# Kernel optimization log

Hardware: AMD Instinct MI355X
Metric: run time of the kernel (lower is better)

The kernel has to match this reference:

```python
import jax, jax.numpy as jnp
import numpy as np

B, T, F, H = 32, 2048, 768, 12
DH = F // H  # 64


def setup_inputs() -> dict:
    key = jax.random.key(0)
    ks = jax.random.split(key, 4)
    x = jax.random.normal(ks[0], (B, T, F), dtype=jnp.float32)
    mask = jnp.zeros((B, 1, T, 1), dtype=jnp.float32)
    W_attn = jax.random.normal(ks[1], (F, 3 * F), dtype=jnp.float32) * 0.02
    b_attn = jnp.zeros((1, 3 * F), dtype=jnp.float32)
    W_proj = jax.random.normal(ks[2], (F, F), dtype=jnp.float32) * 0.02
    b_proj = jnp.zeros((1, F), dtype=jnp.float32)
    return {"x": x, "mask": mask, "W_attn": W_attn, "b_attn": b_attn,
            "W_proj": W_proj, "b_proj": b_proj}


def _split_heads(t):
    # [B, T, F] -> [B, H, T, dh]
    b, s, f = t.shape
    return t.reshape(b, s, H, f // H).transpose(0, 2, 1, 3)


def _merge_heads(t):
    # [B, H, T, dh] -> [B, T, F]
    b, h, s, d = t.shape
    return t.transpose(0, 2, 1, 3).reshape(b, s, h * d)


def reference(x, mask, W_attn, b_attn, W_proj, b_proj):
    qkv = x @ W_attn + b_attn                      # [B, T, 3F]
    q, k, v = jnp.split(qkv, 3, axis=2)
    q, k, v = _split_heads(q), _split_heads(k), _split_heads(v)  # [B,H,T,dh]

    dk = jnp.asarray(DH, jnp.float32)
    # matmul(q, k, transpose_a=True): contract over T -> [B, H, dh, dh]
    w = jnp.einsum('bhtd,bhte->bhde', q, k) / jnp.sqrt(dk)
    # causal mask over feature axis (nd == ns == dh -> lower triangle)
    i = jnp.arange(DH)[:, None]
    j = jnp.arange(DH)[None, :]
    b = (i >= j).astype(w.dtype)                   # [dh, dh]
    w = w * b - 10000.0 * (1.0 - b)
    # matmul(w, v, transpose_b=True): [B,H,dh,dh] @ [B,H,dh,T] -> [B,H,dh,T]
    w = jnp.einsum('bhde,bhte->bhdt', w, v)
    w = w / (dk ** 4)
    w = w.transpose(0, 1, 3, 2)                    # [B, H, T, dh]
    w = w + mask                                   # mask broadcasts [B,1,T,1]
    w = jax.nn.softmax(w, axis=-2)                 # softmax over time axis
    # dropout is identity at inference (training=False)
    a = v * w                                      # elementwise, not matmul

    a = _merge_heads(a)                            # [B, T, F]
    w = _merge_heads(w)                            # [B, T, F]
    a = a @ W_proj + b_proj
    return (a, w)
```

## Files before the change

### kernel.cpp

```cpp
#include <hip/hip_runtime.h>

#define B_    32
#define T_    2048
#define F_    768
#define H_    12
#define DH_   64
#define MTOK  (B_*T_)
#define NQKV  (3*F_)

typedef __bf16 bf16;
typedef __bf16 bf16x8 __attribute__((ext_vector_type(8)));
typedef float  f32x4  __attribute__((ext_vector_type(4)));

__device__ __forceinline__ void gload_lds16(const bf16* g, bf16* l) {
  __builtin_amdgcn_global_load_lds(
      (const __attribute__((address_space(1))) unsigned*)g,
      (__attribute__((address_space(3))) unsigned*)l, 16, 0, 0);
}

__global__ void k_cast_x(const float* __restrict__ in, bf16* __restrict__ out, int n8) {
  int i = blockIdx.x * 256 + threadIdx.x;
  if (i >= n8) return;
  const float4* p = (const float4*)in + (size_t)i * 2;
  float4 f0 = p[0], f1 = p[1];
  bf16x8 o;
  o[0]=(bf16)f0.x; o[1]=(bf16)f0.y; o[2]=(bf16)f0.z; o[3]=(bf16)f0.w;
  o[4]=(bf16)f1.x; o[5]=(bf16)f1.y; o[6]=(bf16)f1.z; o[7]=(bf16)f1.w;
  *((bf16x8*)out + i) = o;
}

__global__ void k_tcast(const float* __restrict__ in, bf16* __restrict__ out, int K, int N) {
  __shared__ float tile[32][33];
  int n0 = blockIdx.x * 32, k0 = blockIdx.y * 32;
  int tx = threadIdx.x & 31, ty = threadIdx.x >> 5;
#pragma unroll
  for (int r = 0; r < 4; ++r)
    tile[ty + r*8][tx] = in[(size_t)(k0 + ty + r*8) * N + n0 + tx];
  __syncthreads();
#pragma unroll
  for (int r = 0; r < 4; ++r)
    out[(size_t)(n0 + ty + r*8) * K + k0 + tx] = (bf16)tile[tx][ty + r*8];
}

template <typename OutT>
__global__ void k_gemm_bt(const bf16* __restrict__ A, const bf16* __restrict__ Bt,
                          const float* __restrict__ bias, OutT* __restrict__ C,
                          int M, int N, int K, int Nt) {
  __shared__ bf16 As[128 * 32];
  __shared__ bf16 Bs[128 * 32];
  int nwg = gridDim.x;
  int bid = blockIdx.x;
  int swz = (bid & 7) * (nwg >> 3) + (bid >> 3);
  int bn = swz % Nt, bm = swz / Nt;
  int tid = threadIdx.x, wv = tid >> 6, l = tid & 63;
  int wm = (wv >> 1) * 64, wn = (wv & 1) * 64;
  f32x4 acc[4][4] = {};
  const bf16* Ab = A + (size_t)(bm * 128) * K;
  const bf16* Bb = Bt + (size_t)(bn * 128) * K;
  int srow = l >> 2;
  int scol = (l & 3) * 8;
  const int nk = K >> 5;
  for (int kt = 0; kt < nk; ++kt) {
    int k0 = kt * 32;
    __syncthreads();
#pragma unroll
    for (int i = 0; i < 2; ++i) {
      int rr = (i * 4 + wv) * 16 + srow;
      gload_lds16(Ab + (size_t)rr * K + k0 + scol, As + (i * 4 + wv) * 512);
      gload_lds16(Bb + (size_t)rr * K + k0 + scol, Bs + (i * 4 + wv) * 512);
    }
    __syncthreads();
    bf16x8 af[4], bfr[4];
#pragma unroll
    for (int t = 0; t < 4; ++t) {
      af[t]  = *(const bf16x8*)&As[(wm + t * 16 + (l & 15)) * 32 + (l >> 4) * 8];
      bfr[t] = *(const bf16x8*)&Bs[(wn + t * 16 + (l & 15)) * 32 + (l >> 4) * 8];
    }
#pragma unroll
    for (int mi = 0; mi < 4; ++mi)
#pragma unroll
      for (int ni = 0; ni < 4; ++ni)
        acc[mi][ni] = __builtin_amdgcn_mfma_f32_16x16x32_bf16(af[mi], bfr[ni], acc[mi][ni], 0, 0, 0);
  }
#pragma unroll
  for (int ni = 0; ni < 4; ++ni) {
    int col = bn * 128 + wn + ni * 16 + (l & 15);
    float bv = bias[col];
#pragma unroll
    for (int mi = 0; mi < 4; ++mi)
#pragma unroll
      for (int r = 0; r < 4; ++r) {
        int row = bm * 128 + wm + mi * 16 + (l >> 4) * 4 + r;
        C[(size_t)row * N + col] = (OutT)(acc[mi][ni][r] + bv);
      }
  }
}

__global__ __launch_bounds__(256) void k_stage2(const bf16* __restrict__ qkv,
                                                bf16* __restrict__ S2b) {
  int bh = blockIdx.x;
  int b = bh / H_, h = bh % H_;
  int tid = threadIdx.x, wv = tid >> 6, l = tid & 63;
  const bf16* qb = qkv + (size_t)b * T_ * NQKV + h * DH_;
  const bf16* kb = qb + F_;
  f32x4 acc[4][4] = {};
  int tbase = wv * 512 + (l >> 4) * 8;
  int dcol = l & 15;
  for (int kt = 0; kt < 16; ++kt) {
    int t0 = tbase + kt * 32;
    bf16x8 af[4], bfv[4];
#pragma unroll
    for (int j = 0; j < 8; ++j) {
      const bf16* qrow = qb + (size_t)(t0 + j) * NQKV;
      const bf16* krow = kb + (size_t)(t0 + j) * NQKV;
#pragma unroll
      for (int di = 0; di < 4; ++di) {
        af[di][j]  = qrow[di * 16 + dcol];
        bfv[di][j] = krow[di * 16 + dcol];
      }
    }
#pragma unroll
    for (int di = 0; di < 4; ++di)
#pragma unroll
      for (int ej = 0; ej < 4; ++ej)
        acc[di][ej] = __builtin_amdgcn_mfma_f32_16x16x32_bf16(af[di], bfv[ej], acc[di][ej], 0, 0, 0);
  }
  __shared__ float Sred[64][68];
  for (int w = 0; w < 4; ++w) {
    if (wv == w) {
#pragma unroll
      for (int di = 0; di < 4; ++di)
#pragma unroll
        for (int ej = 0; ej < 4; ++ej)
#pragma unroll
          for (int r = 0; r < 4; ++r) {
            int d = di * 16 + (l >> 4) * 4 + r;
            int e = ej * 16 + dcol;
            if (w == 0) Sred[d][e] = acc[di][ej][r];
            else        Sred[d][e] += acc[di][ej][r];
          }
    }
    __syncthreads();
  }
  const float sc_keep = 0.125f / 16777216.0f;
  const float sc_mask = -10000.0f / 16777216.0f;
  bf16* out = S2b + (size_t)bh * 4096;
  for (int i = tid; i < 4096; i += 256) {
    int d = i >> 6, e = i & 63;
    float v = (e <= d) ? Sred[d][e] * sc_keep : sc_mask;
    out[i] = (bf16)v;
  }
}

__global__ __launch_bounds__(256) void k_stage3(const bf16* __restrict__ qkv,
                                                const bf16* __restrict__ S2b,
                                                const float* __restrict__ mask,
                                                float* __restrict__ w_out,
                                                bf16* __restrict__ a_pre) {
  int bh = blockIdx.x;
  int b = bh / H_, h = bh % H_;
  int tid = threadIdx.x, wv = tid >> 6, l = tid & 63;
  const bf16* S2 = S2b + (size_t)bh * 4096;
  bf16x8 sfrag[2][4];
#pragma unroll
  for (int ks = 0; ks < 2; ++ks)
#pragma unroll
    for (int n = 0; n < 4; ++n)
      sfrag[ks][n] = *(const bf16x8*)&S2[(n * 16 + (l & 15)) * 64 + ks * 32 + (l >> 4) * 8];
  const bf16* vb = qkv + (size_t)b * T_ * NQKV + 2 * F_ + h * DH_;
  const float* mb = mask + (size_t)b * T_;
  int t_lo = wv * 512;

  float se[4] = {0.f, 0.f, 0.f, 0.f};
  for (int t0 = t_lo; t0 < t_lo + 512; t0 += 16) {
    f32x4 acc[4] = {};
    bf16x8 a0 = *(const bf16x8*)&vb[(size_t)(t0 + (l & 15)) * NQKV + (l >> 4) * 8];
    bf16x8 a1 = *(const bf16x8*)&vb[(size_t)(t0 + (l & 15)) * NQKV + 32 + (l >> 4) * 8];
#pragma unroll
    for (int n = 0; n < 4; ++n) {
      acc[n] = __builtin_amdgcn_mfma_f32_16x16x32_bf16(a0, sfrag[0][n], acc[n], 0, 0, 0);
      acc[n] = __builtin_amdgcn_mfma_f32_16x16x32_bf16(a1, sfrag[1][n], acc[n], 0, 0, 0);
    }
    float4 mv = *(const float4*)&mb[t0 + (l >> 4) * 4];
    float mr[4] = {mv.x, mv.y, mv.z, mv.w};
#pragma unroll
    for (int n = 0; n < 4; ++n)
#pragma unroll
      for (int r = 0; r < 4; ++r)
        se[n] += __expf(acc[n][r] + mr[r]);
  }
#pragma unroll
  for (int n = 0; n < 4; ++n) {
    se[n] += __shfl_xor(se[n], 16, 64);
    se[n] += __shfl_xor(se[n], 32, 64);
  }
  __shared__ float sred[4][64];
  __shared__ float inv[64];
  if (l < 16) {
#pragma unroll
    for (int n = 0; n < 4; ++n) sred[wv][n * 16 + l] = se[n];
  }
  __syncthreads();
  if (tid < 64) inv[tid] = 1.0f / (sred[0][tid] + sred[1][tid] + sred[2][tid] + sred[3][tid]);
  __syncthreads();
  float iv[4];
#pragma unroll
  for (int n = 0; n < 4; ++n) iv[n] = inv[n * 16 + (l & 15)];

  for (int t0 = t_lo; t0 < t_lo + 512; t0 += 16) {
    f32x4 acc[4] = {};
    bf16x8 a0 = *(const bf16x8*)&vb[(size_t)(t0 + (l & 15)) * NQKV + (l >> 4) * 8];
    bf16x8 a1 = *(const bf16x8*)&vb[(size_t)(t0 + (l & 15)) * NQKV + 32 + (l >> 4) * 8];
#pragma unroll
    for (int n = 0; n < 4; ++n) {
      acc[n] = __builtin_amdgcn_mfma_f32_16x16x32_bf16(a0, sfrag[0][n], acc[n], 0, 0, 0);
      acc[n] = __builtin_amdgcn_mfma_f32_16x16x32_bf16(a1, sfrag[1][n], acc[n], 0, 0, 0);
    }
    float4 mv = *(const float4*)&mb[t0 + (l >> 4) * 4];
    float mr[4] = {mv.x, mv.y, mv.z, mv.w};
#pragma unroll
    for (int r = 0; r < 4; ++r) {
      int t = t0 + (l >> 4) * 4 + r;
      size_t orow = ((size_t)b * T_ + t) * F_ + h * DH_;
#pragma unroll
      for (int n = 0; n < 4; ++n) {
        int dd = n * 16 + (l & 15);
        float w = __expf(acc[n][r] + mr[r]) * iv[n];
        w_out[orow + dd] = w;
        float vval = (float)vb[(size_t)t * NQKV + dd];
        a_pre[orow + dd] = (bf16)(vval * w);
      }
    }
  }
}

extern "C" void kernel_launch(void* const* d_in, const int* in_sizes, int n_in,
                              void* d_out, int out_size, void* d_ws, size_t ws_size,
                              hipStream_t stream) {
  const float* x      = (const float*)d_in[0];
  const float* mask   = (const float*)d_in[1];
  const float* W_attn = (const float*)d_in[2];
  const float* b_attn = (const float*)d_in[3];
  const float* W_proj = (const float*)d_in[4];
  const float* b_proj = (const float*)d_in[5];
  float* out_a = (float*)d_out;
  float* out_w = out_a + (size_t)MTOK * F_;

  char* ws = (char*)d_ws;
  bf16*  qkv   = (bf16*)(ws + 0);
  bf16*  xb    = (bf16*)(ws + 301989888ull);
  bf16*  waT   = (bf16*)(ws + 402653184ull);
  bf16*  wpT   = (bf16*)(ws + 406192128ull);
  bf16*  S2b   = (bf16*)(ws + 432537600ull);
  bf16*  a_pre = xb;

  k_cast_x<<<24576, 256, 0, stream>>>(x, xb, MTOK * F_ / 8);
  k_tcast<<<dim3(NQKV / 32, F_ / 32), 256, 0, stream>>>(W_attn, waT, F_, NQKV);
  k_tcast<<<dim3(F_ / 32, F_ / 32), 256, 0, stream>>>(W_proj, wpT, F_, F_);
  k_gemm_bt<bf16><<<(MTOK / 128) * (NQKV / 128), 256, 0, stream>>>(
      xb, waT, b_attn, qkv, MTOK, NQKV, F_, NQKV / 128);
  k_stage2<<<B_ * H_, 256, 0, stream>>>(qkv, S2b);
  k_stage3<<<B_ * H_, 256, 0, stream>>>(qkv, S2b, mask, out_w, a_pre);
  k_gemm_bt<float><<<(MTOK / 128) * (F_ / 128), 256, 0, stream>>>(
      a_pre, wpT, b_proj, out_a, MTOK, F_, F_, F_ / 128);
}
```

Before: 1.169 ms.

## Write Q and K transposed from QKV GEMM and widen attention blocks to 1024 threads

The QKV GEMM epilogue now writes Q and K in a feature-major transposed layout with padded row pitch, and V as a separate compact [tokens, F] buffer. Stage 2 can then load contiguous 8-element vectors along time instead of doing scalar strided gathers. Both attention stages move from 256 to 1024 threads per block so each block has more waves and each wave handles less of the time range. The cost is that the transposed epilogue stores are less coalesced, and stage 2 must reduce partial results from 16 waves through shared memory one wave at a time.

```diff
diff --git a/kernel.cpp b/kernel.cpp
--- a/kernel.cpp
+++ b/kernel.cpp
@@ -7,8 +7,10 @@
 #define DH_   64
 #define MTOK  (B_*T_)
 #define NQKV  (3*F_)
+#define MTP   65600
 
 typedef __bf16 bf16;
+typedef __bf16 bf16x4 __attribute__((ext_vector_type(4)));
 typedef __bf16 bf16x8 __attribute__((ext_vector_type(8)));
 typedef float  f32x4  __attribute__((ext_vector_type(4)));
 
@@ -42,9 +44,75 @@
     out[(size_t)(n0 + ty + r*8) * K + k0 + tx] = (bf16)tile[tx][ty + r*8];
 }
 
-template <typename OutT>
+__global__ void k_gemm_qkv(const bf16* __restrict__ A, const bf16* __restrict__ Bt,
+                           const float* __restrict__ bias,
+                           bf16* __restrict__ qT, bf16* __restrict__ kT,
+                           bf16* __restrict__ vout) {
+  const int K = F_;
+  __shared__ bf16 As[128 * 32];
+  __shared__ bf16 Bs[128 * 32];
+  int nwg = gridDim.x;
+  int bid = blockIdx.x;
+  int swz = (bid & 7) * (nwg >> 3) + (bid >> 3);
+  int bn = swz % 18, bm = swz / 18;
+  int tid = threadIdx.x, wv = tid >> 6, l = tid & 63;
+  int wm = (wv >> 1) * 64, wn = (wv & 1) * 64;
+  f32x4 acc[4][4] = {};
+  const bf16* Ab = A + (size_t)(bm * 128) * K;
+  const bf16* Bb = Bt + (size_t)(bn * 128) * K;
+  int srow = l >> 2, scol = (l & 3) * 8;
+  for (int kt = 0; kt < 24; ++kt) {
+    int k0 = kt * 32;
+    __syncthreads();
+#pragma unroll
+    for (int i = 0; i < 2; ++i) {
+      int rr = (i * 4 + wv) * 16 + srow;
+      gload_lds16(Ab + (size_t)rr * K + k0 + scol, As + (i * 4 + wv) * 512);
+      gload_lds16(Bb + (size_t)rr * K + k0 + scol, Bs + (i * 4 + wv) * 512);
+    }
+    __syncthreads();
+    bf16x8 af[4], bfr[4];
+#pragma unroll
+    for (int t = 0; t < 4; ++t) {
+      af[t]  = *(const bf16x8*)&As[(wm + t * 16 + (l & 15)) * 32 + (l >> 4) * 8];
+      bfr[t] = *(const bf16x8*)&Bs[(wn + t * 16 + (l & 15)) * 32 + (l >> 4) * 8];
+    }
+#pragma unroll
+    for (int mi = 0; mi < 4; ++mi)
+#pragma unroll
+      for (int ni = 0; ni < 4; ++ni)
+        acc[mi][ni] = __builtin_amdgcn_mfma_f32_16x16x32_bf16(af[mi], bfr[ni], acc[mi][ni], 0, 0, 0);
+  }
+#pragma unroll
+  for (int ni = 0; ni < 4; ++ni) {
+    int col = bn * 128 + wn + ni * 16 + (l & 15);
+    float bv = bias[col];
+    if (col < 1536) {
+      bf16* rp = (col < 768) ? (qT + (size_t)col * MTP)
+                             : (kT + (size_t)(col - 768) * MTP);
+#pragma unroll
+      for (int mi = 0; mi < 4; ++mi) {
+        int row0 = bm * 128 + wm + mi * 16 + (l >> 4) * 4;
+        bf16x4 o;
+#pragma unroll
+        for (int r = 0; r < 4; ++r) o[r] = (bf16)(acc[mi][ni][r] + bv);
+        *(bf16x4*)&rp[row0] = o;
+      }
+    } else {
+      int vc = col - 1536;
+#pragma unroll
+      for (int mi = 0; mi < 4; ++mi)
+#pragma unroll
+        for (int r = 0; r < 4; ++r) {
+          int row = bm * 128 + wm + mi * 16 + (l >> 4) * 4 + r;
+          vout[(size_t)row * F_ + vc] = (bf16)(acc[mi][ni][r] + bv);
+        }
+    }
+  }
+}
+
 __global__ void k_gemm_bt(const bf16* __restrict__ A, const bf16* __restrict__ Bt,
-                          const float* __restrict__ bias, OutT* __restrict__ C,
+                          const float* __restrict__ bias, float* __restrict__ C,
                           int M, int N, int K, int Nt) {
   __shared__ bf16 As[128 * 32];
   __shared__ bf16 Bs[128 * 32];
@@ -57,8 +125,7 @@
   f32x4 acc[4][4] = {};
   const bf16* Ab = A + (size_t)(bm * 128) * K;
   const bf16* Bb = Bt + (size_t)(bn * 128) * K;
-  int srow = l >> 2;
-  int scol = (l & 3) * 8;
+  int srow = l >> 2, scol = (l & 3) * 8;
   const int nk = K >> 5;
   for (int kt = 0; kt < nk; ++kt) {
     int k0 = kt * 32;
@@ -91,33 +158,27 @@
 #pragma unroll
       for (int r = 0; r < 4; ++r) {
         int row = bm * 128 + wm + mi * 16 + (l >> 4) * 4 + r;
-        C[(size_t)row * N + col] = (OutT)(acc[mi][ni][r] + bv);
+        C[(size_t)row * N + col] = acc[mi][ni][r] + bv;
       }
   }
 }
 
-__global__ __launch_bounds__(256) void k_stage2(const bf16* __restrict__ qkv,
-                                                bf16* __restrict__ S2b) {
+__global__ __launch_bounds__(1024) void k_stage2(const bf16* __restrict__ qT,
+                                                 const bf16* __restrict__ kT,
+                                                 bf16* __restrict__ S2b) {
   int bh = blockIdx.x;
   int b = bh / H_, h = bh % H_;
   int tid = threadIdx.x, wv = tid >> 6, l = tid & 63;
-  const bf16* qb = qkv + (size_t)b * T_ * NQKV + h * DH_;
-  const bf16* kb = qb + F_;
+  const bf16* qb = qT + (size_t)(h * DH_) * MTP + b * T_;
+  const bf16* kb = kT + (size_t)(h * DH_) * MTP + b * T_;
   f32x4 acc[4][4] = {};
-  int tbase = wv * 512 + (l >> 4) * 8;
-  int dcol = l & 15;
-  for (int kt = 0; kt < 16; ++kt) {
-    int t0 = tbase + kt * 32;
+  for (int kt = 0; kt < 4; ++kt) {
+    int t0 = wv * 128 + kt * 32 + (l >> 4) * 8;
     bf16x8 af[4], bfv[4];
 #pragma unroll
-    for (int j = 0; j < 8; ++j) {
-      const bf16* qrow = qb + (size_t)(t0 + j) * NQKV;
-      const bf16* krow = kb + (size_t)(t0 + j) * NQKV;
-#pragma unroll
-      for (int di = 0; di < 4; ++di) {
-        af[di][j]  = qrow[di * 16 + dcol];
-        bfv[di][j] = krow[di * 16 + dcol];
-      }
+    for (int di = 0; di < 4; ++di) {
+      af[di]  = *(const bf16x8*)&qb[(size_t)(di * 16 + (l & 15)) * MTP + t0];
+      bfv[di] = *(const bf16x8*)&kb[(size_t)(di * 16 + (l & 15)) * MTP + t0];
     }
 #pragma unroll
     for (int di = 0; di < 4; ++di)
@@ -126,7 +187,7 @@
         acc[di][ej] = __builtin_amdgcn_mfma_f32_16x16x32_bf16(af[di], bfv[ej], acc[di][ej], 0, 0, 0);
   }
   __shared__ float Sred[64][68];
-  for (int w = 0; w < 4; ++w) {
+  for (int w = 0; w < 16; ++w) {
     if (wv == w) {
 #pragma unroll
       for (int di = 0; di < 4; ++di)
@@ -135,7 +196,7 @@
 #pragma unroll
           for (int r = 0; r < 4; ++r) {
             int d = di * 16 + (l >> 4) * 4 + r;
-            int e = ej * 16 + dcol;
+            int e = ej * 16 + (l & 15);
             if (w == 0) Sred[d][e] = acc[di][ej][r];
             else        Sred[d][e] += acc[di][ej][r];
           }
@@ -145,18 +206,17 @@
   const float sc_keep = 0.125f / 16777216.0f;
   const float sc_mask = -10000.0f / 16777216.0f;
   bf16* out = S2b + (size_t)bh * 4096;
-  for (int i = tid; i < 4096; i += 256) {
+  for (int i = tid; i < 4096; i += 1024) {
     int d = i >> 6, e = i & 63;
-    float v = (e <= d) ? Sred[d][e] * sc_keep : sc_mask;
-    out[i] = (bf16)v;
-  }
-}
-
-__global__ __launch_bounds__(256) void k_stage3(const bf16* __restrict__ qkv,
-                                                const bf16* __restrict__ S2b,
-                                                const float* __restrict__ mask,
-                                                float* __restrict__ w_out,
-                                                bf16* __restrict__ a_pre) {
+    out[i] = (bf16)((e <= d) ? Sred[d][e] * sc_keep : sc_mask);
+  }
+}
+
+__global__ __launch_bounds__(1024) void k_stage3(const bf16* __restrict__ v,
+                                                 const bf16* __restrict__ S2b,
+                                                 const float* __restrict__ mask,
+                                                 float* __restrict__ w_out,
+                                                 bf16* __restrict__ a_pre) {
   int bh = blockIdx.x;
   int b = bh / H_, h = bh % H_;
   int tid = threadIdx.x, wv = tid >> 6, l = tid & 63;
@@ -167,15 +227,15 @@
 #pragma unroll
     for (int n = 0; n < 4; ++n)
       sfrag[ks][n] = *(const bf16x8*)&S2[(n * 16 + (l & 15)) * 64 + ks * 32 + (l >> 4) * 8];
-  const bf16* vb = qkv + (size_t)b * T_ * NQKV + 2 * F_ + h * DH_;
+  const bf16* vb = v + (size_t)b * T_ * F_ + h * DH_;
   const float* mb = mask + (size_t)b * T_;
-  int t_lo = wv * 512;
+  int t_lo = wv * 128;
 
   float se[4] = {0.f, 0.f, 0.f, 0.f};
-  for (int t0 = t_lo; t0 < t_lo + 512; t0 += 16) {
+  for (int t0 = t_lo; t0 < t_lo + 128; t0 += 16) {
     f32x4 acc[4] = {};
-    bf16x8 a0 = *(const bf16x8*)&vb[(size_t)(t0 + (l & 15)) * NQKV + (l >> 4) * 8];
-    bf16x8 a1 = *(const bf16x8*)&vb[(size_t)(t0 + (l & 15)) * NQKV + 32 + (l >> 4) * 8];
+    bf16x8 a0 = *(const bf16x8*)&vb[(size_t)(t0 + (l & 15)) * F_ + (l >> 4) * 8];
+    bf16x8 a1 = *(const bf16x8*)&vb[(size_t)(t0 + (l & 15)) * F_ + 32 + (l >> 4) * 8];
 #pragma unroll
     for (int n = 0; n < 4; ++n) {
       acc[n] = __builtin_amdgcn_mfma_f32_16x16x32_bf16(a0, sfrag[0][n], acc[n], 0, 0, 0);
@@ -194,23 +254,28 @@
     se[n] += __shfl_xor(se[n], 16, 64);
     se[n] += __shfl_xor(se[n], 32, 64);
   }
-  __shared__ float sred[4][64];
+  __shared__ float sred[16][64];
   __shared__ float inv[64];
   if (l < 16) {
 #pragma unroll
     for (int n = 0; n < 4; ++n) sred[wv][n * 16 + l] = se[n];
   }
   __syncthreads();
-  if (tid < 64) inv[tid] = 1.0f / (sred[0][tid] + sred[1][tid] + sred[2][tid] + sred[3][tid]);
+  if (tid < 64) {
+    float s = 0.f;
+#pragma unroll
+    for (int w = 0; w < 16; ++w) s += sred[w][tid];
+    inv[tid] = 1.0f / s;
+  }
   __syncthreads();
   float iv[4];
 #pragma unroll
   for (int n = 0; n < 4; ++n) iv[n] = inv[n * 16 + (l & 15)];
 
-  for (int t0 = t_lo; t0 < t_lo + 512; t0 += 16) {
+  for (int t0 = t_lo; t0 < t_lo + 128; t0 += 16) {
     f32x4 acc[4] = {};
-    bf16x8 a0 = *(const bf16x8*)&vb[(size_t)(t0 + (l & 15)) * NQKV + (l >> 4) * 8];
-    bf16x8 a1 = *(const bf16x8*)&vb[(size_t)(t0 + (l & 15)) * NQKV + 32 + (l >> 4) * 8];
+    bf16x8 a0 = *(const bf16x8*)&vb[(size_t)(t0 + (l & 15)) * F_ + (l >> 4) * 8];
+    bf16x8 a1 = *(const bf16x8*)&vb[(size_t)(t0 + (l & 15)) * F_ + 32 + (l >> 4) * 8];
 #pragma unroll
     for (int n = 0; n < 4; ++n) {
       acc[n] = __builtin_amdgcn_mfma_f32_16x16x32_bf16(a0, sfrag[0][n], acc[n], 0, 0, 0);
@@ -227,7 +292,7 @@
         int dd = n * 16 + (l & 15);
         float w = __expf(acc[n][r] + mr[r]) * iv[n];
         w_out[orow + dd] = w;
-        float vval = (float)vb[(size_t)t * NQKV + dd];
+        float vval = (float)vb[(size_t)t * F_ + dd];
         a_pre[orow + dd] = (bf16)(vval * w);
       }
     }
@@ -247,20 +312,22 @@
   float* out_w = out_a + (size_t)MTOK * F_;
 
   char* ws = (char*)d_ws;
-  bf16*  qkv   = (bf16*)(ws + 0);
-  bf16*  xb    = (bf16*)(ws + 301989888ull);
-  bf16*  waT   = (bf16*)(ws + 402653184ull);
-  bf16*  wpT   = (bf16*)(ws + 406192128ull);
-  bf16*  S2b   = (bf16*)(ws + 432537600ull);
-  bf16*  a_pre = xb;
+  bf16* xb  = (bf16*)(ws + 0);
+  bf16* qT  = (bf16*)(ws + 100663296ull);
+  bf16* kT  = (bf16*)(ws + 201424896ull);
+  bf16* v   = (bf16*)(ws + 302186496ull);
+  bf16* waT = (bf16*)(ws + 402849792ull);
+  bf16* wpT = (bf16*)(ws + 406388736ull);
+  bf16* S2b = (bf16*)(ws + 407568384ull);
+  bf16* a_pre = xb;
 
   k_cast_x<<<24576, 256, 0, stream>>>(x, xb, MTOK * F_ / 8);
   k_tcast<<<dim3(NQKV / 32, F_ / 32), 256, 0, stream>>>(W_attn, waT, F_, NQKV);
   k_tcast<<<dim3(F_ / 32, F_ / 32), 256, 0, stream>>>(W_proj, wpT, F_, F_);
-  k_gemm_bt<bf16><<<(MTOK / 128) * (NQKV / 128), 256, 0, stream>>>(
-      xb, waT, b_attn, qkv, MTOK, NQKV, F_, NQKV / 128);
-  k_stage2<<<B_ * H_, 256, 0, stream>>>(qkv, S2b);
-  k_stage3<<<B_ * H_, 256, 0, stream>>>(qkv, S2b, mask, out_w, a_pre);
-  k_gemm_bt<float><<<(MTOK / 128) * (F_ / 128), 256, 0, stream>>>(
+  k_gemm_qkv<<<(MTOK / 128) * (NQKV / 128), 256, 0, stream>>>(
+      xb, waT, b_attn, qT, kT, v);
+  k_stage2<<<B_ * H_, 1024, 0, stream>>>(qT, kT, S2b);
+  k_stage3<<<B_ * H_, 1024, 0, stream>>>(v, S2b, mask, out_w, a_pre);
+  k_gemm_bt<<<(MTOK / 128) * (F_ / 128), 256, 0, stream>>>(
       a_pre, wpT, b_proj, out_a, MTOK, F_, F_, F_ / 128);
 }
```

New measurement: 1.145 ms. 2.0% less time.
